# Kernel tuning notes

Hardware: AMD Instinct MI355X
Metric: run time of the kernel (lower is better)

The kernel has to match this reference:

```python
import jax, jax.numpy as jnp
import numpy as np


def _make_pert(r, s):
    lin = np.linspace(-r, r, s)
    xm, ym, tm = np.meshgrid(lin, lin, lin)  # default 'xy' indexing, matches torch code
    return jnp.asarray(np.stack([xm.ravel(), ym.ravel(), tm.ravel()], axis=-1), dtype=jnp.float32)

PERTS = (_make_pert(0.01, 3), _make_pert(0.05, 5), _make_pert(0.09, 7))  # [27,3],[125,3],[343,3]

N, IN, H, HQ, FF, OUT = 4096, 3, 256, 64, 64, 3


def setup_inputs():
    key = jax.random.key(0)
    ks = jax.random.split(key, 24)

    def W(k, i, o):
        return (jax.random.normal(k, (i, o), jnp.float32) / np.sqrt(i)).astype(jnp.float32)

    one = jnp.ones((1,), jnp.float32)
    return {
        "x": jax.random.normal(ks[0], (N, 1), jnp.float32),
        "y": jax.random.normal(ks[1], (N, 1), jnp.float32),
        "t": jax.random.normal(ks[2], (N, 1), jnp.float32),
        # linear_emb: 3 -> 64 -> WaveAct -> 256
        "emb_W1": W(ks[3], IN, HQ), "emb_b1": jnp.zeros((HQ,), jnp.float32),
        "emb_wa": one, "emb_wb": one,
        "emb_W2": W(ks[4], HQ, H), "emb_b2": jnp.zeros((H,), jnp.float32),
        # multiregion_mixer: 4 -> 8 -> WaveAct -> 1
        "mix_W1": W(ks[5], 4, 8), "mix_b1": jnp.zeros((8,), jnp.float32),
        "mix_wa": one, "mix_wb": one,
        "mix_W2": W(ks[6], 8, 1), "mix_b2": jnp.zeros((1,), jnp.float32),
        "out_W0": W(ks[7], H, FF), "out_b0": jnp.zeros((FF,), jnp.float32),
        "out_wa0": one, "out_wb0": one,
        "out_Wh": jnp.stack([W(ks[8 + i], FF, FF) for i in range(3)]),
        "out_bh": jnp.zeros((3, FF), jnp.float32),
        "out_wah": jnp.ones((3, 1), jnp.float32), "out_wbh": jnp.ones((3, 1), jnp.float32),
        "out_Wf1": W(ks[11], FF, FF), "out_bf1": jnp.zeros((FF,), jnp.float32),
        "out_waf": one, "out_wbf": one,
        "out_Wf2": W(ks[12], FF, OUT), "out_bf2": jnp.zeros((OUT,), jnp.float32),
    }


def _wave(h, wa, wb):
    return wa * jnp.sin(h) + wb * jnp.cos(h)


def reference(x, y, t,
              emb_W1, emb_b1, emb_wa, emb_wb, emb_W2, emb_b2,
              mix_W1, mix_b1, mix_wa, mix_wb, mix_W2, mix_b2,
              out_W0, out_b0, out_wa0, out_wb0,
              out_Wh, out_bh, out_wah, out_wbh,
              out_Wf1, out_bf1, out_waf, out_wbf, out_Wf2, out_bf2):
    def emb(s):  # [..., 3] -> [..., 256]
        h = _wave(s @ emb_W1 + emb_b1, emb_wa, emb_wb)
        return h @ emb_W2 + emb_b2

    src = jnp.concatenate([x, y, t], axis=-1)           # [N, 3]
    feats = [emb(src)]                                   # region 1: unperturbed
    for P in PERTS:
        perturbed = src[:, None, :] + P[None, :, :]      # [N, P, 3]
        feats.append(emb(perturbed).mean(axis=1))        # [N, 256]
    stacked = jnp.stack(feats, axis=-1)                  # [N, 256, 4] (== permute(0,2,1) of stack dim=1)

    m = _wave(stacked @ mix_W1 + mix_b1, mix_wa, mix_wb) # [N, 256, 8]
    e = (m @ mix_W2 + mix_b2)[:, :, 0]                   # [N, 256]

    h = _wave(e @ out_W0 + out_b0, out_wa0, out_wb0)     # [N, 64]
    for i in range(3):                                   # fixed num_layer-1 = 3 hidden layers
        h = _wave(h @ out_Wh[i] + out_bh[i], out_wah[i], out_wbh[i])
    h = _wave(h @ out_Wf1 + out_bf1, out_waf, out_wbf)
    return h @ out_Wf2 + out_bf2                         # [N, 3]
```

## Files before the change

kernel.cpp:

```cpp
#include <hip/hip_runtime.h>

#define SPB 4

__global__ __launch_bounds__(256) void model_fused(
    const float* __restrict__ x, const float* __restrict__ y, const float* __restrict__ t,
    const float* __restrict__ embW1, const float* __restrict__ embb1,
    const float* __restrict__ embwa, const float* __restrict__ embwb,
    const float* __restrict__ embW2, const float* __restrict__ embb2,
    const float* __restrict__ mixW1, const float* __restrict__ mixb1,
    const float* __restrict__ mixwa, const float* __restrict__ mixwb,
    const float* __restrict__ mixW2, const float* __restrict__ mixb2,
    const float* __restrict__ outW0, const float* __restrict__ outb0,
    const float* __restrict__ outwa0, const float* __restrict__ outwb0,
    const float* __restrict__ outWh, const float* __restrict__ outbh,
    const float* __restrict__ outwah, const float* __restrict__ outwbh,
    const float* __restrict__ outWf1, const float* __restrict__ outbf1,
    const float* __restrict__ outwaf, const float* __restrict__ outwbf,
    const float* __restrict__ outWf2, const float* __restrict__ outbf2,
    float* __restrict__ out, int N)
{
    __shared__ float sC[3][64];
    __shared__ float sw[SPB][64];
    __shared__ float se[SPB][256];
    __shared__ float sh[2][SPB][64];
    __shared__ float sMixW1[32], sMixb1[8], sMixW2[8];

    const int tid = threadIdx.x;
    const int n0  = blockIdx.x * SPB;

    if (tid < 32)       sMixW1[tid]      = mixW1[tid];
    else if (tid < 40)  sMixb1[tid - 32] = mixb1[tid - 32];
    else if (tid < 48)  sMixW2[tid - 40] = mixW2[tid - 40];

    {
        const int ch = tid & 63;
        const int sm = tid >> 6;
        const float w0 = embW1[ch], w1 = embW1[64 + ch], w2 = embW1[128 + ch];
        if (sm == 0) {
            float ga = (1.f + 2.f*__cosf(0.01f*w0))
                     * (1.f + 2.f*__cosf(0.01f*w1))
                     * (1.f + 2.f*__cosf(0.01f*w2)) * (1.f/27.f);
            float gb = (1.f + 2.f*(__cosf(0.025f*w0) + __cosf(0.05f*w0)))
                     * (1.f + 2.f*(__cosf(0.025f*w1) + __cosf(0.05f*w1)))
                     * (1.f + 2.f*(__cosf(0.025f*w2) + __cosf(0.05f*w2))) * (1.f/125.f);
            float gc = (1.f + 2.f*(__cosf(0.03f*w0) + __cosf(0.06f*w0) + __cosf(0.09f*w0)))
                     * (1.f + 2.f*(__cosf(0.03f*w1) + __cosf(0.06f*w1) + __cosf(0.09f*w1)))
                     * (1.f + 2.f*(__cosf(0.03f*w2) + __cosf(0.06f*w2) + __cosf(0.09f*w2))) * (1.f/343.f);
            sC[0][ch] = ga; sC[1][ch] = gb; sC[2][ch] = gc;
        }
        const int n  = n0 + sm;
        const int ns = (n < N) ? n : (N - 1);
        float u = x[ns]*w0 + y[ns]*w1 + t[ns]*w2 + embb1[ch];
        sw[sm][ch] = embwa[0]*__sinf(u) + embwb[0]*__cosf(u);
    }
    __syncthreads();

    {
        const int c = tid;
        float a0[SPB], a1[SPB], a2[SPB], a3[SPB];
        #pragma unroll
        for (int n = 0; n < SPB; ++n) { a0[n]=0.f; a1[n]=0.f; a2[n]=0.f; a3[n]=0.f; }

        #pragma unroll 4
        for (int ch = 0; ch < 64; ++ch) {
            const float wr = embW2[ch*256 + c];
            const float c1 = sC[0][ch], c2 = sC[1][ch], c3 = sC[2][ch];
            #pragma unroll
            for (int n = 0; n < SPB; ++n) {
                const float tn = sw[n][ch] * wr;
                a0[n] += tn;
                a1[n] = fmaf(tn, c1, a1[n]);
                a2[n] = fmaf(tn, c2, a2[n]);
                a3[n] = fmaf(tn, c3, a3[n]);
            }
        }

        const float mwa = mixwa[0], mwb = mixwb[0], mb2 = mixb2[0];
        const float bb2 = embb2[c];
        #pragma unroll
        for (int n = 0; n < SPB; ++n) {
            const float s0 = a0[n]+bb2, s1 = a1[n]+bb2, s2 = a2[n]+bb2, s3 = a3[n]+bb2;
            float ev = mb2;
            #pragma unroll
            for (int j = 0; j < 8; ++j) {
                float p = fmaf(s0, sMixW1[j],
                          fmaf(s1, sMixW1[8 + j],
                          fmaf(s2, sMixW1[16 + j],
                          fmaf(s3, sMixW1[24 + j], sMixb1[j]))));
                ev = fmaf(mwa*__sinf(p) + mwb*__cosf(p), sMixW2[j], ev);
            }
            se[n][c] = ev;
        }
    }
    __syncthreads();

    const int n = tid >> 6, f = tid & 63;
    {
        float a = outb0[f];
        for (int k = 0; k < 256; ++k)
            a = fmaf(se[n][k], outW0[k*64 + f], a);
        sh[0][n][f] = outwa0[0]*__sinf(a) + outwb0[0]*__cosf(a);
    }
    __syncthreads();

    int cur = 0;
    #pragma unroll
    for (int i = 0; i < 3; ++i) {
        float a = outbh[i*64 + f];
        const float* W = outWh + i*4096;
        #pragma unroll 8
        for (int k = 0; k < 64; ++k)
            a = fmaf(sh[cur][n][k], W[k*64 + f], a);
        sh[1 - cur][n][f] = outwah[i]*__sinf(a) + outwbh[i]*__cosf(a);
        __syncthreads();
        cur ^= 1;
    }
    {
        float a = outbf1[f];
        #pragma unroll 8
        for (int k = 0; k < 64; ++k)
            a = fmaf(sh[cur][n][k], outWf1[k*64 + f], a);
        sh[1 - cur][n][f] = outwaf[0]*__sinf(a) + outwbf[0]*__cosf(a);
        __syncthreads();
        cur ^= 1;
    }
    if (tid < SPB*3) {
        const int nn = tid / 3, o = tid - nn*3;
        float a = outbf2[o];
        #pragma unroll 8
        for (int k = 0; k < 64; ++k)
            a = fmaf(sh[cur][nn][k], outWf2[k*3 + o], a);
        const int gn = n0 + nn;
        if (gn < N) out[gn*3 + o] = a;
    }
}

extern "C" void kernel_launch(void* const* d_in, const int* in_sizes, int n_in,
                              void* d_out, int out_size, void* d_ws, size_t ws_size,
                              hipStream_t stream) {
    const float* x      = (const float*)d_in[0];
    const float* y      = (const float*)d_in[1];
    const float* t      = (const float*)d_in[2];
    const float* embW1  = (const float*)d_in[3];
    const float* embb1  = (const float*)d_in[4];
    const float* embwa  = (const float*)d_in[5];
    const float* embwb  = (const float*)d_in[6];
    const float* embW2  = (const float*)d_in[7];
    const float* embb2  = (const float*)d_in[8];
    const float* mixW1  = (const float*)d_in[9];
    const float* mixb1  = (const float*)d_in[10];
    const float* mixwa  = (const float*)d_in[11];
    const float* mixwb  = (const float*)d_in[12];
    const float* mixW2  = (const float*)d_in[13];
    const float* mixb2  = (const float*)d_in[14];
    const float* outW0  = (const float*)d_in[15];
    const float* outb0  = (const float*)d_in[16];
    const float* outwa0 = (const float*)d_in[17];
    const float* outwb0 = (const float*)d_in[18];
    const float* outWh  = (const float*)d_in[19];
    const float* outbh  = (const float*)d_in[20];
    const float* outwah = (const float*)d_in[21];
    const float* outwbh = (const float*)d_in[22];
    const float* outWf1 = (const float*)d_in[23];
    const float* outbf1 = (const float*)d_in[24];
    const float* outwaf = (const float*)d_in[25];
    const float* outwbf = (const float*)d_in[26];
    const float* outWf2 = (const float*)d_in[27];
    const float* outbf2 = (const float*)d_in[28];
    float* out = (float*)d_out;

    const int N = in_sizes[0];
    const int blocks = (N + SPB - 1) / SPB;
    model_fused<<<blocks, 256, 0, stream>>>(
        x, y, t,
        embW1, embb1, embwa, embwb, embW2, embb2,
        mixW1, mixb1, mixwa, mixwb, mixW2, mixb2,
        outW0, outb0, outwa0, outwb0,
        outWh, outbh, outwah, outwbh,
        outWf1, outbf1, outwaf, outwbf, outWf2, outbf2,
        out, N);
}
```

Measured before the change: 140.5 us.

## Rewrite fused model with fp16 MFMA matmuls and pre-transposed weights

Adds a preprocess kernel that transposes and converts the weight matrices to fp16 in workspace and precomputes the per-channel perturbation mean factors. The main kernel now handles 16 samples per block and runs the embedding, output and hidden-layer matmuls with 16x16x32 fp16 MFMA instructions, staging W2 into padded shared memory. This replaces scalar FP32 FMA loops and cuts the block count, at the cost of fp16 rounding of weights and activations, an extra launch, and a larger per-block shared-memory copy.

```diff
diff --git a/kernel.cpp b/kernel.cpp
--- a/kernel.cpp
+++ b/kernel.cpp
@@ -1,136 +1,200 @@
 #include <hip/hip_runtime.h>
 
-#define SPB 4
-
-__global__ __launch_bounds__(256) void model_fused(
+typedef _Float16 f16;
+typedef _Float16 f16x8 __attribute__((ext_vector_type(8)));
+typedef float v4f __attribute__((ext_vector_type(4)));
+
+#define WS_W2T  0
+#define WS_W0T  16384
+#define WS_WHT  32768
+#define WS_WF1T 45056
+#define WS_CDW  24576
+
+__global__ __launch_bounds__(256) void preprocess(
+    const float* __restrict__ embW1, const float* __restrict__ embW2,
+    const float* __restrict__ outW0, const float* __restrict__ outWh,
+    const float* __restrict__ outWf1, f16* __restrict__ wsh)
+{
+    const int g = blockIdx.x * 256 + threadIdx.x;
+    if (g < 16384) {
+        const int c = g >> 6, k = g & 63;
+        wsh[WS_W2T + g] = (f16)embW2[k*256 + c];
+    } else if (g < 32768) {
+        const int i = g - 16384;
+        const int f = i >> 8, k = i & 255;
+        wsh[WS_W0T + i] = (f16)outW0[k*64 + f];
+    } else if (g < 45056) {
+        const int i = g - 32768;
+        const int l = i >> 12, f = (i >> 6) & 63, k = i & 63;
+        wsh[WS_WHT + i] = (f16)outWh[l*4096 + k*64 + f];
+    } else if (g < 49152) {
+        const int i = g - 45056;
+        const int f = i >> 6, k = i & 63;
+        wsh[WS_WF1T + i] = (f16)outWf1[k*64 + f];
+    } else if (g < 49344) {
+        const int i = g - 49152;
+        const int r = i >> 6, ch = i & 63;
+        const float w0 = embW1[ch], w1 = embW1[64 + ch], w2 = embW1[128 + ch];
+        float v;
+        if (r == 0) {
+            v = (1.f + 2.f*__cosf(0.01f*w0)) * (1.f + 2.f*__cosf(0.01f*w1))
+              * (1.f + 2.f*__cosf(0.01f*w2)) * (1.f/27.f);
+        } else if (r == 1) {
+            v = (1.f + 2.f*(__cosf(0.025f*w0) + __cosf(0.05f*w0)))
+              * (1.f + 2.f*(__cosf(0.025f*w1) + __cosf(0.05f*w1)))
+              * (1.f + 2.f*(__cosf(0.025f*w2) + __cosf(0.05f*w2))) * (1.f/125.f);
+        } else {
+            v = (1.f + 2.f*(__cosf(0.03f*w0) + __cosf(0.06f*w0) + __cosf(0.09f*w0)))
+              * (1.f + 2.f*(__cosf(0.03f*w1) + __cosf(0.06f*w1) + __cosf(0.09f*w1)))
+              * (1.f + 2.f*(__cosf(0.03f*w2) + __cosf(0.06f*w2) + __cosf(0.09f*w2))) * (1.f/343.f);
+        }
+        ((float*)wsh)[WS_CDW + i] = v;
+    }
+}
+
+__global__ __launch_bounds__(256) void model_mfma(
     const float* __restrict__ x, const float* __restrict__ y, const float* __restrict__ t,
     const float* __restrict__ embW1, const float* __restrict__ embb1,
     const float* __restrict__ embwa, const float* __restrict__ embwb,
-    const float* __restrict__ embW2, const float* __restrict__ embb2,
+    const float* __restrict__ embb2,
     const float* __restrict__ mixW1, const float* __restrict__ mixb1,
     const float* __restrict__ mixwa, const float* __restrict__ mixwb,
     const float* __restrict__ mixW2, const float* __restrict__ mixb2,
-    const float* __restrict__ outW0, const float* __restrict__ outb0,
+    const float* __restrict__ outb0,
     const float* __restrict__ outwa0, const float* __restrict__ outwb0,
-    const float* __restrict__ outWh, const float* __restrict__ outbh,
+    const float* __restrict__ outbh,
     const float* __restrict__ outwah, const float* __restrict__ outwbh,
-    const float* __restrict__ outWf1, const float* __restrict__ outbf1,
+    const float* __restrict__ outbf1,
     const float* __restrict__ outwaf, const float* __restrict__ outwbf,
     const float* __restrict__ outWf2, const float* __restrict__ outbf2,
+    const f16* __restrict__ wsh,
     float* __restrict__ out, int N)
 {
-    __shared__ float sC[3][64];
-    __shared__ float sw[SPB][64];
-    __shared__ float se[SPB][256];
-    __shared__ float sh[2][SPB][64];
-    __shared__ float sMixW1[32], sMixb1[8], sMixW2[8];
-
-    const int tid = threadIdx.x;
-    const int n0  = blockIdx.x * SPB;
-
-    if (tid < 32)       sMixW1[tid]      = mixW1[tid];
-    else if (tid < 40)  sMixb1[tid - 32] = mixb1[tid - 32];
-    else if (tid < 48)  sMixW2[tid - 40] = mixW2[tid - 40];
-
-    {
-        const int ch = tid & 63;
-        const int sm = tid >> 6;
-        const float w0 = embW1[ch], w1 = embW1[64 + ch], w2 = embW1[128 + ch];
-        if (sm == 0) {
-            float ga = (1.f + 2.f*__cosf(0.01f*w0))
-                     * (1.f + 2.f*__cosf(0.01f*w1))
-                     * (1.f + 2.f*__cosf(0.01f*w2)) * (1.f/27.f);
-            float gb = (1.f + 2.f*(__cosf(0.025f*w0) + __cosf(0.05f*w0)))
-                     * (1.f + 2.f*(__cosf(0.025f*w1) + __cosf(0.05f*w1)))
-                     * (1.f + 2.f*(__cosf(0.025f*w2) + __cosf(0.05f*w2))) * (1.f/125.f);
-            float gc = (1.f + 2.f*(__cosf(0.03f*w0) + __cosf(0.06f*w0) + __cosf(0.09f*w0)))
-                     * (1.f + 2.f*(__cosf(0.03f*w1) + __cosf(0.06f*w1) + __cosf(0.09f*w1)))
-                     * (1.f + 2.f*(__cosf(0.03f*w2) + __cosf(0.06f*w2) + __cosf(0.09f*w2))) * (1.f/343.f);
-            sC[0][ch] = ga; sC[1][ch] = gb; sC[2][ch] = gc;
-        }
-        const int n  = n0 + sm;
-        const int ns = (n < N) ? n : (N - 1);
-        float u = x[ns]*w0 + y[ns]*w1 + t[ns]*w2 + embb1[ch];
-        sw[sm][ch] = embwa[0]*__sinf(u) + embwb[0]*__cosf(u);
+    __shared__ __attribute__((aligned(16))) f16 sW2T[256*72];
+    __shared__ __attribute__((aligned(16))) f16 sA[64*72];
+    __shared__ __attribute__((aligned(16))) f16 sE[16*264];
+    __shared__ __attribute__((aligned(16))) f16 sH[2][16*72];
+    __shared__ float sHf[16*65];
+
+    const int tid  = threadIdx.x;
+    const int lane = tid & 63;
+    const int wv   = tid >> 6;
+    const int n0   = blockIdx.x * 16;
+
+    {
+        const uint4* src = (const uint4*)(wsh + WS_W2T + tid*64);
+        uint4* dst = (uint4*)(sW2T + tid*72);
+        #pragma unroll
+        for (int i = 0; i < 8; ++i) dst[i] = src[i];
+    }
+
+    {
+        const int k = tid & 63;
+        const int sq = tid >> 6;
+        const float w0 = embW1[k], w1 = embW1[64+k], w2 = embW1[128+k];
+        const float b1 = embb1[k];
+        const float ewa = embwa[0], ewb = embwb[0];
+        const float* Cw = (const float*)wsh + WS_CDW;
+        const float c1 = Cw[k], c2 = Cw[64+k], c3 = Cw[128+k];
+        #pragma unroll
+        for (int q = 0; q < 4; ++q) {
+            const int s = sq*4 + q;
+            const int ns = (n0 + s < N) ? (n0 + s) : (N - 1);
+            const float u = fmaf(x[ns], w0, fmaf(y[ns], w1, fmaf(t[ns], w2, b1)));
+            const float sv = ewa*__sinf(u) + ewb*__cosf(u);
+            f16* row = sA + (s*4)*72 + k;
+            row[0]   = (f16)sv;
+            row[72]  = (f16)(sv*c1);
+            row[144] = (f16)(sv*c2);
+            row[216] = (f16)(sv*c3);
+        }
     }
     __syncthreads();
 
-    {
-        const int c = tid;
-        float a0[SPB], a1[SPB], a2[SPB], a3[SPB];
-        #pragma unroll
-        for (int n = 0; n < SPB; ++n) { a0[n]=0.f; a1[n]=0.f; a2[n]=0.f; a3[n]=0.f; }
-
-        #pragma unroll 4
-        for (int ch = 0; ch < 64; ++ch) {
-            const float wr = embW2[ch*256 + c];
-            const float c1 = sC[0][ch], c2 = sC[1][ch], c3 = sC[2][ch];
-            #pragma unroll
-            for (int n = 0; n < SPB; ++n) {
-                const float tn = sw[n][ch] * wr;
-                a0[n] += tn;
-                a1[n] = fmaf(tn, c1, a1[n]);
-                a2[n] = fmaf(tn, c2, a2[n]);
-                a3[n] = fmaf(tn, c3, a3[n]);
-            }
-        }
-
-        const float mwa = mixwa[0], mwb = mixwb[0], mb2 = mixb2[0];
-        const float bb2 = embb2[c];
-        #pragma unroll
-        for (int n = 0; n < SPB; ++n) {
-            const float s0 = a0[n]+bb2, s1 = a1[n]+bb2, s2 = a2[n]+bb2, s3 = a3[n]+bb2;
-            float ev = mb2;
+    const int l15 = lane & 15, qb = lane >> 4;
+
+    {
+        const f16x8 af0 = *(const f16x8*)(sA + (16*wv + l15)*72 + qb*8);
+        const f16x8 af1 = *(const f16x8*)(sA + (16*wv + l15)*72 + 32 + qb*8);
+        const int s_loc = 4*wv + qb;
+        const float mwa = mixwa[0], mwb = mixwb[0], mb2v = mixb2[0];
+        #pragma unroll
+        for (int nt = 0; nt < 16; ++nt) {
+            const f16x8 bf0 = *(const f16x8*)(sW2T + (16*nt + l15)*72 + qb*8);
+            const f16x8 bf1 = *(const f16x8*)(sW2T + (16*nt + l15)*72 + 32 + qb*8);
+            v4f acc = {0.f, 0.f, 0.f, 0.f};
+            acc = __builtin_amdgcn_mfma_f32_16x16x32_f16(af0, bf0, acc, 0, 0, 0);
+            acc = __builtin_amdgcn_mfma_f32_16x16x32_f16(af1, bf1, acc, 0, 0, 0);
+            const int c = 16*nt + l15;
+            const float b2c = embb2[c];
+            const float s0 = acc[0]+b2c, s1 = acc[1]+b2c, s2 = acc[2]+b2c, s3 = acc[3]+b2c;
+            float ev = mb2v;
             #pragma unroll
             for (int j = 0; j < 8; ++j) {
-                float p = fmaf(s0, sMixW1[j],
-                          fmaf(s1, sMixW1[8 + j],
-                          fmaf(s2, sMixW1[16 + j],
-                          fmaf(s3, sMixW1[24 + j], sMixb1[j]))));
-                ev = fmaf(mwa*__sinf(p) + mwb*__cosf(p), sMixW2[j], ev);
+                float p = fmaf(s0, mixW1[j],
+                          fmaf(s1, mixW1[8+j],
+                          fmaf(s2, mixW1[16+j],
+                          fmaf(s3, mixW1[24+j], mixb1[j]))));
+                ev = fmaf(mwa*__sinf(p) + mwb*__cosf(p), mixW2[j], ev);
             }
-            se[n][c] = ev;
+            sE[s_loc*264 + c] = (f16)ev;
         }
     }
     __syncthreads();
 
-    const int n = tid >> 6, f = tid & 63;
-    {
-        float a = outb0[f];
-        for (int k = 0; k < 256; ++k)
-            a = fmaf(se[n][k], outW0[k*64 + f], a);
-        sh[0][n][f] = outwa0[0]*__sinf(a) + outwb0[0]*__cosf(a);
+    const int fme = 16*wv + l15;
+
+    {
+        v4f acc = {0.f, 0.f, 0.f, 0.f};
+        const f16* Ae   = sE + l15*264 + qb*8;
+        const f16* W0Tg = wsh + WS_W0T + fme*256 + qb*8;
+        #pragma unroll
+        for (int kt = 0; kt < 8; ++kt) {
+            const f16x8 af = *(const f16x8*)(Ae + kt*32);
+            const f16x8 bf = *(const f16x8*)(W0Tg + kt*32);
+            acc = __builtin_amdgcn_mfma_f32_16x16x32_f16(af, bf, acc, 0, 0, 0);
+        }
+        const float b0 = outb0[fme], wa = outwa0[0], wb = outwb0[0];
+        #pragma unroll
+        for (int r = 0; r < 4; ++r) {
+            const float a = acc[r] + b0;
+            sH[0][(qb*4 + r)*72 + fme] = (f16)(wa*__sinf(a) + wb*__cosf(a));
+        }
     }
     __syncthreads();
 
     int cur = 0;
     #pragma unroll
-    for (int i = 0; i < 3; ++i) {
-        float a = outbh[i*64 + f];
-        const float* W = outWh + i*4096;
-        #pragma unroll 8
-        for (int k = 0; k < 64; ++k)
-            a = fmaf(sh[cur][n][k], W[k*64 + f], a);
-        sh[1 - cur][n][f] = outwah[i]*__sinf(a) + outwbh[i]*__cosf(a);
+    for (int i = 0; i < 4; ++i) {
+        const f16* Wg = (i < 3) ? (wsh + WS_WHT + i*4096) : (wsh + WS_WF1T);
+        v4f acc = {0.f, 0.f, 0.f, 0.f};
+        #pragma unroll
+        for (int kt = 0; kt < 2; ++kt) {
+            const f16x8 af = *(const f16x8*)(sH[cur] + l15*72 + kt*32 + qb*8);
+            const f16x8 bf = *(const f16x8*)(Wg + fme*64 + kt*32 + qb*8);
+            acc = __builtin_amdgcn_mfma_f32_16x16x32_f16(af, bf, acc, 0, 0, 0);
+        }
+        float bias, wa, wb;
+        if (i < 3) { bias = outbh[i*64 + fme]; wa = outwah[i]; wb = outwbh[i]; }
+        else       { bias = outbf1[fme];       wa = outwaf[0]; wb = outwbf[0]; }
+        #pragma unroll
+        for (int r = 0; r < 4; ++r) {
+            const float a = acc[r] + bias;
+            const float v = wa*__sinf(a) + wb*__cosf(a);
+            if (i < 3) sH[cur^1][(qb*4 + r)*72 + fme] = (f16)v;
+            else       sHf[(qb*4 + r)*65 + fme] = v;
+        }
         __syncthreads();
         cur ^= 1;
     }
-    {
-        float a = outbf1[f];
-        #pragma unroll 8
+
+    if (tid < 48) {
+        const int s = tid / 3, o = tid - s*3;
+        float a = outbf2[o];
+        #pragma unroll 16
         for (int k = 0; k < 64; ++k)
-            a = fmaf(sh[cur][n][k], outWf1[k*64 + f], a);
-        sh[1 - cur][n][f] = outwaf[0]*__sinf(a) + outwbf[0]*__cosf(a);
-        __syncthreads();
-        cur ^= 1;
-    }
-    if (tid < SPB*3) {
-        const int nn = tid / 3, o = tid - nn*3;
-        float a = outbf2[o];
-        #pragma unroll 8
-        for (int k = 0; k < 64; ++k)
-            a = fmaf(sh[cur][nn][k], outWf2[k*3 + o], a);
-        const int gn = n0 + nn;
+            a = fmaf(sHf[s*65 + k], outWf2[k*3 + o], a);
+        const int gn = n0 + s;
         if (gn < N) out[gn*3 + o] = a;
     }
 }
@@ -168,15 +232,19 @@
     const float* outWf2 = (const float*)d_in[27];
     const float* outbf2 = (const float*)d_in[28];
     float* out = (float*)d_out;
+    f16* wsh = (f16*)d_ws;
 
     const int N = in_sizes[0];
-    const int blocks = (N + SPB - 1) / SPB;
-    model_fused<<<blocks, 256, 0, stream>>>(
+
+    preprocess<<<193, 256, 0, stream>>>(embW1, embW2, outW0, outWh, outWf1, wsh);
+
+    const int blocks = (N + 15) / 16;
+    model_mfma<<<blocks, 256, 0, stream>>>(
         x, y, t,
-        embW1, embb1, embwa, embwb, embW2, embb2,
+        embW1, embb1, embwa, embwb, embb2,
         mixW1, mixb1, mixwa, mixwb, mixW2, mixb2,
-        outW0, outb0, outwa0, outwb0,
-        outWh, outbh, outwah, outwbh,
-        outWf1, outbf1, outwaf, outwbf, outWf2, outbf2,
-        out, N);
+        outb0, outwa0, outwb0,
+        outbh, outwah, outwbh,
+        outbf1, outwaf, outwbf, outWf2, outbf2,
+        wsh, out, N);
 }
```

Result: faster. 126.2 us (-10.1%).
